# Performance work log

Hardware: AMD Instinct MI355X
Metric: run time of the kernel (lower is better)

## Reference

```python
import jax, jax.numpy as jnp
import numpy as np

K = 20
EPS = 1e-5
SLOPE = 0.2


def knn_idx(x, k):
    # x: (B, C, N) -> neighbor indices (B, N, k) by smallest squared distance
    xx = jnp.sum(x * x, axis=1)                      # (B, N)
    inner = jnp.einsum('bcn,bcm->bnm', x, x)         # (B, N, N)
    neg_dist = 2.0 * inner - xx[:, :, None] - xx[:, None, :]
    return jax.lax.top_k(neg_dist, k)[1]             # (B, N, k)


def bn_lrelu(y, g, b, axes):
    # training-mode BatchNorm (batch stats) + LeakyReLU(0.2); channel = last axis
    m = jnp.mean(y, axis=axes, keepdims=True)
    v = jnp.var(y, axis=axes, keepdims=True)
    y = (y - m) * jax.lax.rsqrt(v + EPS) * g + b
    return jnp.where(y > 0, y, SLOPE * y)


def edge_block(x, W, g, b, k):
    # x: (B, C, N); W: (out, 2C). Returns (B, N, out) = max over k neighbors.
    idx = knn_idx(x, k)                              # (B, N, k)
    xt = jnp.transpose(x, (0, 2, 1))                 # (B, N, C)
    feat = jax.vmap(lambda a, i: a[i])(xt, idx)      # (B, N, k, C) gather
    ctr = jnp.broadcast_to(xt[:, :, None, :], feat.shape)
    e = jnp.concatenate([feat - ctr, ctr], axis=-1)  # (B, N, k, 2C)
    y = jnp.einsum('bnkc,oc->bnko', e, W)            # 1x1 conv
    y = bn_lrelu(y, g, b, (0, 1, 2))
    return jnp.max(y, axis=2)                        # (B, N, out)


def setup_inputs() -> dict:
    key = jax.random.key(0)
    ks = jax.random.split(key, 7)
    feat_dims = [64, 64, 128, 256]
    in_dims = [2 * 3, 2 * 64, 2 * 64, 2 * 128]
    B, N = 8, 1024
    d = {'x': jax.random.normal(ks[0], (B, N, 3), dtype=jnp.float32)}
    for i, (ci, co) in enumerate(zip(in_dims, feat_dims)):
        d[f'W{i}'] = jax.random.normal(ks[i + 1], (co, ci), dtype=jnp.float32) * (1.0 / np.sqrt(ci))
        d[f'g{i}'] = jnp.ones((co,), dtype=jnp.float32)
        d[f'b{i}'] = jnp.zeros((co,), dtype=jnp.float32)
    fuse, emb = sum(feat_dims), 1024
    d['Wf'] = jax.random.normal(ks[5], (emb, fuse), dtype=jnp.float32) * (1.0 / np.sqrt(fuse))
    d['gf'] = jnp.ones((emb,), dtype=jnp.float32)
    d['bf'] = jnp.zeros((emb,), dtype=jnp.float32)
    return d


def reference(x, W0, g0, b0, W1, g1, b1, W2, g2, b2, W3, g3, b3, Wf, gf, bf):
    # x: (B, N, 3) -> (B, N, emb)
    h = jnp.transpose(x, (0, 2, 1))                  # (B, 3, N)
    states = []
    for (W, g, b) in [(W0, g0, b0), (W1, g1, b1), (W2, g2, b2), (W3, g3, b3)]:
        hn = edge_block(h, W, g, b, K)               # (B, N, out)
        states.append(hn)
        h = jnp.transpose(hn, (0, 2, 1))             # (B, out, N)
    fused = jnp.concatenate(states, axis=-1)         # (B, N, 512)
    y = jnp.einsum('bnc,oc->bno', fused, Wf)         # final 1x1 conv
    y = bn_lrelu(y, gf, bf, (0, 1))
    return y
```

## Files before the change

### kernel.cpp

```cpp
#include <hip/hip_runtime.h>
#include <math.h>

#define TILE 64
#define KC 16

typedef __attribute__((ext_vector_type(8))) short short8;
typedef __attribute__((ext_vector_type(4))) float float4v;
typedef const __attribute__((address_space(1))) void* gptr_t;
typedef __attribute__((address_space(3))) void* lptr_t;

#define OFF_DF    0ull
#define OFF_PT    0ull
#define OFF_YMAX  16777216ull
#define OFF_YMIN  25165824ull
#define OFF_YF    0ull
#define OFF_IDX   67108864ull
#define OFF_H     67764224ull
#define OFF_FUSB  76152832ull
#define OFF_WFB   84541440ull
#define OFF_XX    85590016ull
#define OFF_WCAT  85655552ull
#define OFF_STATS 85917696ull
#define OFF_COEF  85942272ull

__device__ __forceinline__ unsigned short f2bf(float f) {
  unsigned int u = __float_as_uint(f);
  unsigned int r = (u + 0x7fffu + ((u >> 16) & 1u)) >> 16;
  return (unsigned short)r;
}

__device__ __forceinline__ void gemm_tile_loop(
    const float* __restrict__ A, const float* __restrict__ Bw,
    int K, int lda, int ldb, int rowBase, int colBase,
    float acc[4][4], float* As, float* Bs)
{
  const int tid = threadIdx.x;
  const int tx = tid & 15, ty = tid >> 4;
  for (int k0 = 0; k0 < K; k0 += KC) {
    for (int l = 0; l < 4; ++l) {
      int flat = tid * 4 + l;
      int kk = flat & (KC - 1);
      int row = flat >> 4;
      int gk = k0 + kk;
      float av = 0.f, bv = 0.f;
      if (gk < K) {
        av = A[(size_t)(rowBase + row) * lda + gk];
        bv = Bw[(size_t)(colBase + row) * ldb + gk];
      }
      As[kk * TILE + row] = av;
      Bs[kk * TILE + row] = bv;
    }
    __syncthreads();
#pragma unroll
    for (int kk = 0; kk < KC; ++kk) {
      float a0[4], b0[4];
#pragma unroll
      for (int i = 0; i < 4; ++i) a0[i] = As[kk * TILE + ty * 4 + i];
#pragma unroll
      for (int j = 0; j < 4; ++j) b0[j] = Bs[kk * TILE + tx * 4 + j];
#pragma unroll
      for (int i = 0; i < 4; ++i)
#pragma unroll
        for (int j = 0; j < 4; ++j)
          acc[i][j] = fmaf(a0[i], b0[j], acc[i][j]);
    }
    __syncthreads();
  }
}

__global__ __launch_bounds__(256) void xxf_kernel(const float* __restrict__ H, int C,
                                                  float* __restrict__ xx) {
  int m = blockIdx.x * 256 + threadIdx.x;
  if (m < 8192) {
    float s = 0.f;
    for (int c = 0; c < C; ++c) { float h = H[(size_t)m * C + c]; s = fmaf(h, h, s); }
    xx[m] = s;
  }
}

__global__ __launch_bounds__(256) void distf_kernel(const float* __restrict__ H, int C,
                                                    const float* __restrict__ xx,
                                                    float* __restrict__ Df) {
  __shared__ float As[KC * TILE], Bs[KC * TILE];
  int bz = blockIdx.z;
  int rowBase = bz * 1024 + blockIdx.y * 64;
  int colBase = bz * 1024 + blockIdx.x * 64;
  float acc[4][4] = {};
  gemm_tile_loop(H, H, C, C, C, rowBase, colBase, acc, As, Bs);
  int tx = threadIdx.x & 15, ty = threadIdx.x >> 4;
#pragma unroll
  for (int i = 0; i < 4; ++i) {
    int grow = rowBase + ty * 4 + i;
    float xi = xx[grow];
#pragma unroll
    for (int j = 0; j < 4; ++j) {
      int gj = blockIdx.x * 64 + tx * 4 + j;
      float v = 2.0f * acc[i][j] - xi - xx[colBase + tx * 4 + j];
      Df[(size_t)grow * 1024 + gj] = v;
    }
  }
}

template<int C>
__global__ __launch_bounds__(256) void topk_rerank(const float* __restrict__ Df,
                                                   const float* __restrict__ H,
                                                   int* __restrict__ idx) {
  __shared__ int    candLds[4][64];
  __shared__ double ndLds[4][64];
  __shared__ int    colLds[4][64];
  const int lane = threadIdx.x & 63;
  const int w = threadIdx.x >> 6;
  const int row = blockIdx.x * 4 + w;
  const int b = row >> 10;
  const float* drow = Df + (size_t)row * 1024;

  unsigned s[16];
#pragma unroll
  for (int t = 0; t < 16; ++t) {
    unsigned u = __float_as_uint(drow[lane + 64 * t]);
    s[t] = (u & 0x80000000u) ? ~u : (u | 0x80000000u);
  }

  unsigned p = 0;
  for (int bit = 31; bit >= 0; --bit) {
    unsigned cand = p | (1u << bit);
    int c = 0;
#pragma unroll
    for (int t = 0; t < 16; ++t) c += (s[t] > cand) ? 1 : 0;
#pragma unroll
    for (int off = 1; off < 64; off <<= 1) c += __shfl_xor(c, off, 64);
    if (c >= 32) {
      p = cand;
      if (c <= 64) break;
    }
  }

  int k = 0;
#pragma unroll
  for (int t = 0; t < 16; ++t) k += (s[t] > p) ? 1 : 0;
  int incl = k;
#pragma unroll
  for (int off = 1; off < 64; off <<= 1) {
    int v = __shfl_up(incl, off, 64);
    if (lane >= off) incl += v;
  }
  int slot = incl - k;
#pragma unroll
  for (int t = 0; t < 16; ++t) {
    if (s[t] > p) {
      if (slot < 64) candLds[w][slot] = lane + 64 * t;
      ++slot;
    }
  }
  int nsel = __shfl(incl, 63, 64);
  if (nsel > 64) nsel = 64;

  double nd; int col;
  if (lane < nsel) {
    col = candLds[w][lane];
    const float* xi = H + (size_t)row * C;
    const float* xj = H + (size_t)(b * 1024 + col) * C;
    double ssum = 0.0;
    if (C == 3) {
#pragma unroll
      for (int c = 0; c < 3; ++c) {
        double d = (double)xi[c] - (double)xj[c];
        ssum = fma(d, d, ssum);
      }
    } else {
      for (int c = 0; c < C; c += 4) {
        float4v a = *(const float4v*)(xi + c);
        float4v bb = *(const float4v*)(xj + c);
        double d0 = (double)a.x - (double)bb.x;
        double d1 = (double)a.y - (double)bb.y;
        double d2 = (double)a.z - (double)bb.z;
        double d3 = (double)a.w - (double)bb.w;
        ssum = fma(d0, d0, ssum); ssum = fma(d1, d1, ssum);
        ssum = fma(d2, d2, ssum); ssum = fma(d3, d3, ssum);
      }
    }
    nd = -ssum;
  } else {
    nd = -INFINITY; col = 100000 + lane;
  }
  ndLds[w][lane] = nd;
  colLds[w][lane] = col;

  int rank = 0;
#pragma unroll 4
  for (int j = 0; j < 64; ++j) {
    double vj = ndLds[w][j];
    int cj = colLds[w][j];
    rank += (vj > nd || (vj == nd && cj < col)) ? 1 : 0;
  }
  if (rank < 20) idx[(size_t)row * 20 + rank] = col;
}

__global__ __launch_bounds__(256) void wcat_kernel(const float* __restrict__ W,
                                                   float* __restrict__ Wcat, int outc, int C) {
  int i = blockIdx.x * 256 + threadIdx.x;
  if (i < outc * C) {
    int o = i / C, c = i % C;
    float w1 = W[(size_t)o * 2 * C + c];
    float w2 = W[(size_t)o * 2 * C + C + c];
    Wcat[(size_t)o * C + c] = w1;
    Wcat[(size_t)(outc + o) * C + c] = w2 - w1;
  }
}

__global__ __launch_bounds__(256) void pt_gemm(const float* __restrict__ A,
                                               const float* __restrict__ Bw,
                                               float* __restrict__ Out, int K, int Nn) {
  __shared__ float As[KC * TILE], Bs[KC * TILE];
  int rowBase = blockIdx.y * 64, colBase = blockIdx.x * 64;
  float acc[4][4] = {};
  gemm_tile_loop(A, Bw, K, K, K, rowBase, colBase, acc, As, Bs);
  int tx = threadIdx.x & 15, ty = threadIdx.x >> 4;
#pragma unroll
  for (int i = 0; i < 4; ++i)
#pragma unroll
    for (int j = 0; j < 4; ++j)
      Out[(size_t)(rowBase + ty * 4 + i) * Nn + colBase + tx * 4 + j] = acc[i][j];
}

__global__ __launch_bounds__(256) void edge_reduce(const float* __restrict__ PT,
                                                   const int* __restrict__ idx,
                                                   float* __restrict__ ymax, float* __restrict__ ymin,
                                                   double* __restrict__ sum, double* __restrict__ sumsq,
                                                   int outc, int l2) {
  __shared__ int sidx[16 * 20];
  __shared__ float ssum[256], ssq[256];
  int tid = threadIdx.x;
  int base = blockIdx.x * 16;
  for (int i = tid; i < 320; i += 256) sidx[i] = idx[base * 20 + i];
  __syncthreads();
  int o = tid & (outc - 1);
  int rs = tid >> l2;
  int R = 256 >> l2;
  int twoc = 2 * outc;
  float ls = 0.f, lq = 0.f;
  for (int r = rs; r < 16; r += R) {
    int m = base + r;
    int boff = (m >> 10) << 10;
    float tv = PT[(size_t)m * twoc + outc + o];
    float vmax = -INFINITY, vmin = INFINITY;
#pragma unroll
    for (int k = 0; k < 20; ++k) {
      int nb = sidx[r * 20 + k];
      float p = PT[(size_t)(boff + nb) * twoc + o];
      float y = p + tv;
      vmax = fmaxf(vmax, y);
      vmin = fminf(vmin, y);
      ls += y;
      lq = fmaf(y, y, lq);
    }
    ymax[(size_t)m * outc + o] = vmax;
    ymin[(size_t)m * outc + o] = vmin;
  }
  ssum[tid] = ls; ssq[tid] = lq;
  __syncthreads();
  if (tid < outc) {
    float s = ssum[tid], q = ssq[tid];
    for (int rr = 1; rr < R; ++rr) { s += ssum[tid + rr * outc]; q += ssq[tid + rr * outc]; }
    atomicAdd(&sum[tid], (double)s);
    atomicAdd(&sumsq[tid], (double)q);
  }
}

__global__ __launch_bounds__(256) void coef_kernel(const double* __restrict__ sum,
                                                   const double* __restrict__ sumsq,
                                                   const float* __restrict__ g,
                                                   const float* __restrict__ b,
                                                   float* __restrict__ cA, float* __restrict__ cC,
                                                   int outc, double count) {
  int o = blockIdx.x * 256 + threadIdx.x;
  if (o < outc) {
    double mean = sum[o] / count;
    double var = sumsq[o] / count - mean * mean;
    double a = (double)g[o] / sqrt(var + 1e-5);
    cA[o] = (float)a;
    cC[o] = (float)((double)b[o] - mean * a);
  }
}

__global__ __launch_bounds__(256) void edge_epi(const float* __restrict__ ymax,
                                                const float* __restrict__ ymin,
                                                const float* __restrict__ cA, const float* __restrict__ cC,
                                                float* __restrict__ Hout, unsigned short* __restrict__ fusedb,
                                                int outc, int l2, int choff) {
  int i = blockIdx.x * 256 + threadIdx.x;
  int m = i >> l2;
  int o = i & (outc - 1);
  float a = cA[o], c = cC[o];
  float v = (a >= 0.f) ? ymax[i] : ymin[i];
  float y = fmaf(a, v, c);
  y = (y > 0.f) ? y : 0.2f * y;
  Hout[i] = y;
  fusedb[(size_t)m * 512 + choff + o] = f2bf(y);
}

__global__ __launch_bounds__(256) void cvt_bf16(const float* __restrict__ in,
                                                unsigned short* __restrict__ out, int n) {
  int i = blockIdx.x * 256 + threadIdx.x;
  if (i < n) out[i] = f2bf(in[i]);
}

__global__ __launch_bounds__(256) void final_gemm_mfma(const unsigned short* __restrict__ A,
                                                       const unsigned short* __restrict__ B,
                                                       float* __restrict__ C) {
  __shared__ unsigned short As[128 * 32];
  __shared__ unsigned short Bs[128 * 32];
  const int tid = threadIdx.x;
  const int lane = tid & 63;
  const int w = tid >> 6;
  const int wm = w >> 1, wn = w & 1;
  const int rowBase = blockIdx.y * 128;
  const int colBase = blockIdx.x * 128;
  const int quad = lane >> 4;
  const int l15 = lane & 15;

  float4v acc[4][4] = {};

  for (int k0 = 0; k0 < 512; k0 += 32) {
#pragma unroll
    for (int q = 0; q < 2; ++q) {
      int ch = (w * 2 + q) * 64 + lane;
      int r = ch >> 2, cp = ch & 3;
      const unsigned short* ga = A + (size_t)(rowBase + r) * 512 + k0 + cp * 8;
      const unsigned short* gb = B + (size_t)(colBase + r) * 512 + k0 + cp * 8;
      __builtin_amdgcn_global_load_lds((gptr_t)ga, (lptr_t)(As + (size_t)(w * 2 + q) * 512), 16, 0, 0);
      __builtin_amdgcn_global_load_lds((gptr_t)gb, (lptr_t)(Bs + (size_t)(w * 2 + q) * 512), 16, 0, 0);
    }
    __syncthreads();
    short8 af[4], bf[4];
#pragma unroll
    for (int mi = 0; mi < 4; ++mi)
      af[mi] = *(const short8*)(As + (wm * 64 + mi * 16 + l15) * 32 + quad * 8);
#pragma unroll
    for (int ni = 0; ni < 4; ++ni)
      bf[ni] = *(const short8*)(Bs + (wn * 64 + ni * 16 + l15) * 32 + quad * 8);
#pragma unroll
    for (int mi = 0; mi < 4; ++mi)
#pragma unroll
      for (int ni = 0; ni < 4; ++ni)
        acc[mi][ni] = __builtin_amdgcn_mfma_f32_16x16x32_bf16(af[mi], bf[ni], acc[mi][ni], 0, 0, 0);
    __syncthreads();
  }
#pragma unroll
  for (int mi = 0; mi < 4; ++mi)
#pragma unroll
    for (int ni = 0; ni < 4; ++ni)
#pragma unroll
      for (int r = 0; r < 4; ++r) {
        int gm = rowBase + wm * 64 + mi * 16 + quad * 4 + r;
        int gn = colBase + wn * 64 + ni * 16 + l15;
        C[(size_t)gm * 1024 + gn] = acc[mi][ni][r];
      }
}

__global__ __launch_bounds__(256) void col_stats(const float* __restrict__ yf,
                                                 double* __restrict__ sum, double* __restrict__ sumsq) {
  int col = blockIdx.x * 256 + threadIdx.x;
  int r0 = blockIdx.y * 128;
  float s = 0.f, q = 0.f;
  for (int r = 0; r < 128; ++r) {
    float v = yf[(size_t)(r0 + r) * 1024 + col];
    s += v;
    q = fmaf(v, v, q);
  }
  atomicAdd(&sum[col], (double)s);
  atomicAdd(&sumsq[col], (double)q);
}

__global__ __launch_bounds__(256) void final_epi(const float* __restrict__ yf,
                                                 const float* __restrict__ cA, const float* __restrict__ cC,
                                                 float* __restrict__ out) {
  int i = blockIdx.x * 256 + threadIdx.x;
  int o = i & 1023;
  float y = fmaf(cA[o], yf[i], cC[o]);
  out[i] = (y > 0.f) ? y : 0.2f * y;
}

extern "C" void kernel_launch(void* const* d_in, const int* in_sizes, int n_in,
                              void* d_out, int out_size, void* d_ws, size_t ws_size,
                              hipStream_t stream) {
  const float* x = (const float*)d_in[0];
  const float* W[4]  = {(const float*)d_in[1], (const float*)d_in[4], (const float*)d_in[7], (const float*)d_in[10]};
  const float* g[4]  = {(const float*)d_in[2], (const float*)d_in[5], (const float*)d_in[8], (const float*)d_in[11]};
  const float* bb[4] = {(const float*)d_in[3], (const float*)d_in[6], (const float*)d_in[9], (const float*)d_in[12]};
  const float* Wf  = (const float*)d_in[13];
  const float* gf  = (const float*)d_in[14];
  const float* bfp = (const float*)d_in[15];
  float* out = (float*)d_out;

  char* ws = (char*)d_ws;
  float*  Df    = (float*)(ws + OFF_DF);
  float*  PT    = (float*)(ws + OFF_PT);
  float*  ymax  = (float*)(ws + OFF_YMAX);
  float*  ymin  = (float*)(ws + OFF_YMIN);
  float*  yf    = (float*)(ws + OFF_YF);
  int*    idxb  = (int*)(ws + OFF_IDX);
  float*  Hbuf  = (float*)(ws + OFF_H);
  unsigned short* fusedb = (unsigned short*)(ws + OFF_FUSB);
  unsigned short* wfb    = (unsigned short*)(ws + OFF_WFB);
  float*  xxb   = (float*)(ws + OFF_XX);
  float*  wcat  = (float*)(ws + OFF_WCAT);
  double* stats = (double*)(ws + OFF_STATS);
  float*  coefb = (float*)(ws + OFF_COEF);

  hipMemsetAsync(stats, 0, 24576, stream);
  cvt_bf16<<<(524288 + 255) / 256, 256, 0, stream>>>(Wf, wfb, 524288);

  const int Cin[4]   = {3, 64, 64, 128};
  const int Cout[4]  = {64, 64, 128, 256};
  const int choff[4] = {0, 64, 128, 256};
  const float* Hin = x;
  size_t soff = 0, coff = 0;

  for (int i = 0; i < 4; ++i) {
    int C = Cin[i], oc = Cout[i];
    int l2 = (oc == 64) ? 6 : (oc == 128) ? 7 : 8;
    double* sum = stats + soff;  double* sumsq = sum + oc;  soff += 2 * (size_t)oc;
    float* cA = coefb + coff;    float* cC = cA + oc;       coff += 2 * (size_t)oc;

    xxf_kernel<<<32, 256, 0, stream>>>(Hin, C, xxb);
    distf_kernel<<<dim3(16, 16, 8), 256, 0, stream>>>(Hin, C, xxb, Df);
    if (C == 3)       topk_rerank<3><<<2048, 256, 0, stream>>>(Df, Hin, idxb);
    else if (C == 64) topk_rerank<64><<<2048, 256, 0, stream>>>(Df, Hin, idxb);
    else              topk_rerank<128><<<2048, 256, 0, stream>>>(Df, Hin, idxb);
    wcat_kernel<<<(oc * C + 255) / 256, 256, 0, stream>>>(W[i], wcat, oc, C);
    pt_gemm<<<dim3(2 * oc / 64, 128), 256, 0, stream>>>(Hin, wcat, PT, C, 2 * oc);
    edge_reduce<<<512, 256, 0, stream>>>(PT, idxb, ymax, ymin, sum, sumsq, oc, l2);
    coef_kernel<<<1, 256, 0, stream>>>(sum, sumsq, g[i], bb[i], cA, cC, oc, 163840.0);
    edge_epi<<<(8192 * oc) / 256, 256, 0, stream>>>(ymax, ymin, cA, cC, Hbuf, fusedb, oc, l2, choff[i]);
    Hin = Hbuf;
  }

  double* sumF = stats + soff;  double* sumsqF = sumF + 1024;
  float* cAF = coefb + coff;    float* cCF = cAF + 1024;
  final_gemm_mfma<<<dim3(8, 64), 256, 0, stream>>>(fusedb, wfb, yf);
  col_stats<<<dim3(4, 64), 256, 0, stream>>>(yf, sumF, sumsqF);
  coef_kernel<<<4, 256, 0, stream>>>(sumF, sumsqF, gf, bfp, cAF, cCF, 1024, 8192.0);
  final_epi<<<8192 * 1024 / 256, 256, 0, stream>>>(yf, cAF, cCF, out);
}
```

Measured before the change: 637.8 us.

## Compute kNN distance matrix with split-bf16 MFMA instead of FP32 FMA tiles

Replaces the FP32 scalar-FMA pairwise inner-product GEMM with a bf16 MFMA kernel. A new pass first splits each feature into high and low bf16 parts, and three MFMA products (hi*hi, hi*lo, lo*hi) recover near-FP32 accuracy. Tiles are 128x128 and filled with global_load_lds. This adds a split pass and extra workspace and gives slightly lower precision, which the downstream top-k rerank must tolerate.

```diff
diff --git a/kernel.cpp b/kernel.cpp
--- a/kernel.cpp
+++ b/kernel.cpp
@@ -22,6 +22,8 @@
 #define OFF_WCAT  85655552ull
 #define OFF_STATS 85917696ull
 #define OFF_COEF  85942272ull
+#define OFF_HHI   85954560ull
+#define OFF_HLO   88051712ull
 
 __device__ __forceinline__ unsigned short f2bf(float f) {
   unsigned int u = __float_as_uint(f);
@@ -78,27 +80,89 @@
   }
 }
 
-__global__ __launch_bounds__(256) void distf_kernel(const float* __restrict__ H, int C,
-                                                    const float* __restrict__ xx,
-                                                    float* __restrict__ Df) {
-  __shared__ float As[KC * TILE], Bs[KC * TILE];
-  int bz = blockIdx.z;
-  int rowBase = bz * 1024 + blockIdx.y * 64;
-  int colBase = bz * 1024 + blockIdx.x * 64;
-  float acc[4][4] = {};
-  gemm_tile_loop(H, H, C, C, C, rowBase, colBase, acc, As, Bs);
-  int tx = threadIdx.x & 15, ty = threadIdx.x >> 4;
-#pragma unroll
-  for (int i = 0; i < 4; ++i) {
-    int grow = rowBase + ty * 4 + i;
-    float xi = xx[grow];
-#pragma unroll
-    for (int j = 0; j < 4; ++j) {
-      int gj = blockIdx.x * 64 + tx * 4 + j;
-      float v = 2.0f * acc[i][j] - xi - xx[colBase + tx * 4 + j];
-      Df[(size_t)grow * 1024 + gj] = v;
-    }
-  }
+__global__ __launch_bounds__(256) void split_bf16(const float* __restrict__ H, int C, int l2kp,
+                                                  unsigned short* __restrict__ hi,
+                                                  unsigned short* __restrict__ lo) {
+  int i = blockIdx.x * 256 + threadIdx.x;
+  int m = i >> l2kp;
+  int c = i & ((1 << l2kp) - 1);
+  unsigned short h = 0, l = 0;
+  if (c < C) {
+    float v = H[(size_t)m * C + c];
+    h = f2bf(v);
+    float hf = __uint_as_float((unsigned)h << 16);
+    l = f2bf(v - hf);
+  }
+  hi[i] = h;
+  lo[i] = l;
+}
+
+__global__ __launch_bounds__(256) void dist_mfma(const unsigned short* __restrict__ Hhi,
+                                                 const unsigned short* __restrict__ Hlo,
+                                                 const float* __restrict__ xx,
+                                                 float* __restrict__ Df, int Kp) {
+  __shared__ unsigned short Ash[128 * 32], Asl[128 * 32];
+  __shared__ unsigned short Bsh[128 * 32], Bsl[128 * 32];
+  const int tid = threadIdx.x;
+  const int lane = tid & 63;
+  const int w = tid >> 6;
+  const int wm = w >> 1, wn = w & 1;
+  const int bz = blockIdx.z;
+  const int rowBase = bz * 1024 + blockIdx.y * 128;
+  const int colBase = bz * 1024 + blockIdx.x * 128;
+  const int quad = lane >> 4;
+  const int l15 = lane & 15;
+
+  float4v acc[4][4] = {};
+
+  for (int k0 = 0; k0 < Kp; k0 += 32) {
+#pragma unroll
+    for (int q = 0; q < 2; ++q) {
+      int ch = (w * 2 + q) * 64 + lane;
+      int r = ch >> 2, cp = ch & 3;
+      size_t offA = (size_t)(rowBase + r) * Kp + k0 + cp * 8;
+      size_t offB = (size_t)(colBase + r) * Kp + k0 + cp * 8;
+      int seg = (w * 2 + q) * 512;
+      __builtin_amdgcn_global_load_lds((gptr_t)(Hhi + offA), (lptr_t)(Ash + seg), 16, 0, 0);
+      __builtin_amdgcn_global_load_lds((gptr_t)(Hlo + offA), (lptr_t)(Asl + seg), 16, 0, 0);
+      __builtin_amdgcn_global_load_lds((gptr_t)(Hhi + offB), (lptr_t)(Bsh + seg), 16, 0, 0);
+      __builtin_amdgcn_global_load_lds((gptr_t)(Hlo + offB), (lptr_t)(Bsl + seg), 16, 0, 0);
+    }
+    __syncthreads();
+    short8 ah[4], al[4], bh[4], bl[4];
+#pragma unroll
+    for (int mi = 0; mi < 4; ++mi) {
+      int ro = (wm * 64 + mi * 16 + l15) * 32 + quad * 8;
+      ah[mi] = *(const short8*)(Ash + ro);
+      al[mi] = *(const short8*)(Asl + ro);
+    }
+#pragma unroll
+    for (int ni = 0; ni < 4; ++ni) {
+      int ro = (wn * 64 + ni * 16 + l15) * 32 + quad * 8;
+      bh[ni] = *(const short8*)(Bsh + ro);
+      bl[ni] = *(const short8*)(Bsl + ro);
+    }
+#pragma unroll
+    for (int mi = 0; mi < 4; ++mi)
+#pragma unroll
+      for (int ni = 0; ni < 4; ++ni) {
+        acc[mi][ni] = __builtin_amdgcn_mfma_f32_16x16x32_bf16(ah[mi], bh[ni], acc[mi][ni], 0, 0, 0);
+        acc[mi][ni] = __builtin_amdgcn_mfma_f32_16x16x32_bf16(ah[mi], bl[ni], acc[mi][ni], 0, 0, 0);
+        acc[mi][ni] = __builtin_amdgcn_mfma_f32_16x16x32_bf16(al[mi], bh[ni], acc[mi][ni], 0, 0, 0);
+      }
+    __syncthreads();
+  }
+#pragma unroll
+  for (int mi = 0; mi < 4; ++mi)
+#pragma unroll
+    for (int ni = 0; ni < 4; ++ni)
+#pragma unroll
+      for (int r = 0; r < 4; ++r) {
+        int gm = rowBase + wm * 64 + mi * 16 + quad * 4 + r;
+        int gn = blockIdx.x * 128 + wn * 64 + ni * 16 + l15;
+        float v = 2.0f * acc[mi][ni][r] - xx[gm] - xx[bz * 1024 + gn];
+        Df[(size_t)gm * 1024 + gn] = v;
+      }
 }
 
 template<int C>
@@ -407,6 +471,8 @@
   float*  wcat  = (float*)(ws + OFF_WCAT);
   double* stats = (double*)(ws + OFF_STATS);
   float*  coefb = (float*)(ws + OFF_COEF);
+  unsigned short* hhi = (unsigned short*)(ws + OFF_HHI);
+  unsigned short* hlo = (unsigned short*)(ws + OFF_HLO);
 
   hipMemsetAsync(stats, 0, 24576, stream);
   cvt_bf16<<<(524288 + 255) / 256, 256, 0, stream>>>(Wf, wfb, 524288);
@@ -420,11 +486,14 @@
   for (int i = 0; i < 4; ++i) {
     int C = Cin[i], oc = Cout[i];
     int l2 = (oc == 64) ? 6 : (oc == 128) ? 7 : 8;
+    int Kp = (C == 3) ? 32 : C;
+    int l2kp = (Kp == 32) ? 5 : (Kp == 64) ? 6 : 7;
     double* sum = stats + soff;  double* sumsq = sum + oc;  soff += 2 * (size_t)oc;
     float* cA = coefb + coff;    float* cC = cA + oc;       coff += 2 * (size_t)oc;
 
     xxf_kernel<<<32, 256, 0, stream>>>(Hin, C, xxb);
-    distf_kernel<<<dim3(16, 16, 8), 256, 0, stream>>>(Hin, C, xxb, Df);
+    split_bf16<<<(8192 << l2kp) / 256, 256, 0, stream>>>(Hin, C, l2kp, hhi, hlo);
+    dist_mfma<<<dim3(8, 8, 8), 256, 0, stream>>>(hhi, hlo, xxb, Df, Kp);
     if (C == 3)       topk_rerank<3><<<2048, 256, 0, stream>>>(Df, Hin, idxb);
     else if (C == 64) topk_rerank<64><<<2048, 256, 0, stream>>>(Df, Hin, idxb);
     else              topk_rerank<128><<<2048, 256, 0, stream>>>(Df, Hin, idxb);
```

Result: faster. 536.8 us (-15.8%).
